# Optimization experiments

Hardware: AMD Instinct MI355X
Metric: run time of the kernel (lower is better)

The kernel has to match this reference:

```python
import jax, jax.numpy as jnp
import numpy as np

# Fixed hyperparameters (from init_kwargs)
GRID_H, GRID_W = 31, 51
PAD = min(GRID_H, GRID_W) - 1          # 30
KSIZE = 2 * PAD + 1                     # 61
FWHM = 13.0
IN_H, IN_W = 1080, 1920                 # input_shape
OUT_H, OUT_W = 1080, 1920               # output_shape
BANDWIDTH_SCALE = 1.0
AMPLITUDE_SCALE = 1.0
UNIFORM_BIAS = 1.0 / (KSIZE ** 2)       # 1/(2*pad+1)^2 added to saliency


def _gauss1d():
    x = np.arange(KSIZE, dtype=np.float64)
    c = KSIZE // 2
    return np.exp(-4.0 * np.log(2.0) * (x - c) ** 2 / FWHM ** 2).astype(np.float32)


def _bbox2sal_single(bboxes):
    # bboxes: [m, 4] in xyxy -> saliency [GRID_H, GRID_W]
    wh = bboxes[:, 2:] - bboxes[:, :2]                  # [m,2] box width/height
    cxy = bboxes[:, :2] + 0.5 * wh                      # [m,2] box centers
    widths = wh[:, 0:1] * BANDWIDTH_SCALE               # [m,1]
    heights = wh[:, 1:2] * BANDWIDTH_SCALE              # [m,1]
    xs = jnp.linspace(0.0, float(IN_W), GRID_W)
    ys = jnp.linspace(0.0, float(IN_H), GRID_H)
    X, Y = jnp.meshgrid(xs, ys, indexing='ij')          # [GRID_W, GRID_H] (torch default meshgrid)
    gx = X.ravel()[None, :]                             # [1, n], n = GRID_W*GRID_H
    gy = Y.ravel()[None, :]
    # Mahalanobis-style squared distance per box/grid-point
    dist = (cxy[:, 0:1] - gx) ** 2 / widths + (cxy[:, 1:2] - gy) ** 2 / heights
    sal = jnp.exp(-0.5 * dist)                          # [m, n]
    sal = AMPLITUDE_SCALE * sal / (1e-05 + sal.sum(axis=1, keepdims=True))
    sal = sal + UNIFORM_BIAS
    sal = sal.sum(axis=0)                               # [n]
    sal = sal / sal.sum()
    return sal.reshape(GRID_W, GRID_H).T                # [GRID_H, GRID_W]


def _conv1d_valid(x, f):
    # x: [B, 1, L], f: [K] -> [B, 1, L-K+1]  (cross-correlation; filter is symmetric)
    return jax.lax.conv_general_dilated(
        x, f[None, None, :], window_strides=(1,), padding='VALID',
        dimension_numbers=('NCH', 'OIH', 'NCH'))


def _resize_bilinear_align_corners(x, oh, ow):
    # x: [B, C, h, w] -> [B, C, oh, ow], align_corners=True
    B, C, h, w = x.shape
    ys = jnp.linspace(0.0, h - 1.0, oh)
    xs = jnp.linspace(0.0, w - 1.0, ow)
    y0 = jnp.floor(ys).astype(jnp.int32)
    x0 = jnp.floor(xs).astype(jnp.int32)
    y1 = jnp.minimum(y0 + 1, h - 1)
    x1 = jnp.minimum(x0 + 1, w - 1)
    ty = (ys - y0).astype(x.dtype)
    tx = (xs - x0).astype(x.dtype)
    v = x[:, :, y0, :] * (1.0 - ty)[None, None, :, None] + x[:, :, y1, :] * ty[None, None, :, None]
    v = v[:, :, :, x0] * (1.0 - tx) + v[:, :, :, x1] * tx
    return v


def setup_inputs() -> dict:
    key = jax.random.key(0)
    k1, k2, k3, k4 = jax.random.split(key, 4)
    B, NB = 16, 20
    imgs = jax.random.normal(k1, (B, 3, IN_H, IN_W), dtype=jnp.float32)
    x1 = jax.random.uniform(k2, (B, NB, 1), minval=0.0, maxval=IN_W * 0.7)
    y1 = jax.random.uniform(k3, (B, NB, 1), minval=0.0, maxval=IN_H * 0.7)
    wh = jax.random.uniform(k4, (B, NB, 2), minval=40.0, maxval=300.0)
    gt_bboxes = jnp.concatenate([x1, y1, x1 + wh[..., 0:1], y1 + wh[..., 1:2]], axis=-1)
    return {"imgs": imgs, "gt_bboxes": gt_bboxes.astype(jnp.float32)}


def reference(imgs, gt_bboxes):
    filt = jnp.asarray(_gauss1d())
    saliency = jax.vmap(_bbox2sal_single)(gt_bboxes)    # [B, GRID_H, GRID_W]
    saliency = saliency[:, None, :, :]                  # [B, 1, gh, gw]
    x_sal = saliency.sum(axis=2)                        # [B, 1, gw]
    y_sal = saliency.sum(axis=3)                        # [B, 1, gh]
    x_pad = jnp.pad(x_sal, ((0, 0), (0, 0), (PAD, PAD)), mode='reflect')
    y_pad = jnp.pad(y_sal, ((0, 0), (0, 0), (PAD, PAD)), mode='reflect')
    P_x = (jnp.arange(GRID_W + 2 * PAD, dtype=jnp.float32) - PAD) / (GRID_W - 1.0)
    P_y = (jnp.arange(GRID_H + 2 * PAD, dtype=jnp.float32) - PAD) / (GRID_H - 1.0)
    wx = _conv1d_valid(x_pad, filt)                     # [B, 1, gw]
    ox = _conv1d_valid(P_x[None, None, :] * x_pad, filt)
    xgrid = jnp.clip(ox / wx * 2.0 - 1.0, -1.0, 1.0)    # [B, 1, gw]
    wy = _conv1d_valid(y_pad, filt)                     # [B, 1, gh]
    oy = _conv1d_valid(P_y[None, None, :] * y_pad, filt)
    ygrid = jnp.clip(oy / wy * 2.0 - 1.0, -1.0, 1.0)    # [B, 1, gh]
    B = imgs.shape[0]
    xg = jnp.broadcast_to(xgrid[:, :, None, :], (B, 1, GRID_H, GRID_W))
    yg = jnp.broadcast_to(ygrid[:, :, :, None], (B, 1, GRID_H, GRID_W))
    grid = jnp.concatenate([xg, yg], axis=1)            # [B, 2, gh, gw]
    grid = _resize_bilinear_align_corners(grid, OUT_H, OUT_W)
    return jnp.transpose(grid, (0, 2, 3, 1))            # [B, OUT_H, OUT_W, 2]
```

## Files before the change

### kernel.cpp

```cpp
#include <hip/hip_runtime.h>

#define GH 31
#define GW 51
#define PADc 30
#define KS 61
#define NPTS (GH * GW)

#define NEG4LN2 (-2.7725887222397812f)

__global__ __launch_bounds__(256) void kde_lines(const float* __restrict__ bboxes,
                                                 int NB,
                                                 float* __restrict__ grids) {
    const int b = blockIdx.x;
    const int tid = threadIdx.x;

    __shared__ float salf[NPTS];
    __shared__ float tmp[NPTS];
    __shared__ float red[256];
    __shared__ float xsal[GW], ysal[GH];
    __shared__ float xpad[GW + 2 * PADc];
    __shared__ float ypad[GH + 2 * PADc];
    __shared__ float boxsh[4 * 32];

    for (int i = tid; i < NB * 4; i += 256) boxsh[i] = bboxes[b * NB * 4 + i];
    const float bias0 = (float)NB * (1.0f / ((float)KS * (float)KS));
    for (int g = tid; g < NPTS; g += 256) salf[g] = bias0;
    __syncthreads();

    for (int k = 0; k < NB; ++k) {
        const float x1 = boxsh[k * 4 + 0], y1 = boxsh[k * 4 + 1];
        const float x2 = boxsh[k * 4 + 2], y2 = boxsh[k * 4 + 3];
        const float w = x2 - x1, h = y2 - y1;
        const float cx = x1 + 0.5f * w, cy = y1 + 0.5f * h;
        const float iw = 1.0f / w, ih = 1.0f / h;
        float local = 0.0f;
        for (int g = tid; g < NPTS; g += 256) {
            const int xi = g / GH;
            const int yi = g - xi * GH;
            const float gx = (float)xi * (1920.0f / 50.0f);
            const float gy = (float)yi * (1080.0f / 30.0f);
            const float dx = cx - gx, dy = cy - gy;
            const float d = dx * dx * iw + dy * dy * ih;
            const float e = expf(-0.5f * d);
            tmp[g] = e;
            local += e;
        }
        red[tid] = local;
        __syncthreads();
        for (int s = 128; s > 0; s >>= 1) {
            if (tid < s) red[tid] += red[tid + s];
            __syncthreads();
        }
        const float scale = 1.0f / (1e-5f + red[0]);
        __syncthreads();
        for (int g = tid; g < NPTS; g += 256) salf[g] += tmp[g] * scale;
        __syncthreads();
    }

    if (tid < GW) {
        float s = 0.0f;
        for (int yi = 0; yi < GH; ++yi) s += salf[tid * GH + yi];
        xsal[tid] = s;
    } else if (tid >= 64 && tid < 64 + GH) {
        const int yi = tid - 64;
        float s = 0.0f;
        for (int xi = 0; xi < GW; ++xi) s += salf[xi * GH + yi];
        ysal[yi] = s;
    }
    __syncthreads();

    for (int p = tid; p < GW + 2 * PADc; p += 256) {
        int q = p - PADc;
        if (q < 0) q = -q;
        if (q > GW - 1) q = 2 * (GW - 1) - q;
        xpad[p] = xsal[q];
    }
    for (int p = tid; p < GH + 2 * PADc; p += 256) {
        int q = p - PADc;
        if (q < 0) q = -q;
        if (q > GH - 1) q = 2 * (GH - 1) - q;
        ypad[p] = ysal[q];
    }
    __syncthreads();

    float* og = grids + b * 128;
    if (tid < GW) {
        float wx = 0.0f, ox = 0.0f;
        for (int k2 = 0; k2 < KS; ++k2) {
            const float dk = (float)(k2 - 30);
            const float f = expf(NEG4LN2 * dk * dk * (1.0f / 169.0f));
            const float v = xpad[tid + k2];
            wx += v * f;
            const float P = (float)(tid + k2 - 30) * (1.0f / 50.0f);
            ox += P * v * f;
        }
        float g = ox / wx * 2.0f - 1.0f;
        g = fminf(1.0f, fmaxf(-1.0f, g));
        og[tid] = g;
    } else if (tid >= 64 && tid < 64 + GH) {
        const int j = tid - 64;
        float wy = 0.0f, oy = 0.0f;
        for (int k2 = 0; k2 < KS; ++k2) {
            const float dk = (float)(k2 - 30);
            const float f = expf(NEG4LN2 * dk * dk * (1.0f / 169.0f));
            const float v = ypad[j + k2];
            wy += v * f;
            const float P = (float)(j + k2 - 30) * (1.0f / 30.0f);
            oy += P * v * f;
        }
        float g = oy / wy * 2.0f - 1.0f;
        g = fminf(1.0f, fmaxf(-1.0f, g));
        og[64 + j] = g;
    }
}

__global__ __launch_bounds__(256) void kde_fill(const float* __restrict__ grids,
                                                float4* __restrict__ out, int N4) {
    const int idx = blockIdx.x * 256 + threadIdx.x;
    if (idx >= N4) return;
    const int i = idx % 960;
    const int row = idx / 960;
    const int y = row % 1080;
    const int b = row / 1080;
    const float* og = grids + b * 128;

    const float fy = (float)y * (30.0f / 1079.0f);
    int y0 = (int)fy;
    if (y0 > GH - 1) y0 = GH - 1;
    int y1i = y0 + 1;
    if (y1i > GH - 1) y1i = GH - 1;
    const float ty = fy - (float)y0;
    const float yv = og[64 + y0] * (1.0f - ty) + og[64 + y1i] * ty;

    float xv[2];
#pragma unroll
    for (int p = 0; p < 2; ++p) {
        const int xo = 2 * i + p;
        const float fx = (float)xo * (50.0f / 1919.0f);
        int x0 = (int)fx;
        if (x0 > GW - 1) x0 = GW - 1;
        int x1i = x0 + 1;
        if (x1i > GW - 1) x1i = GW - 1;
        const float tx = fx - (float)x0;
        xv[p] = og[x0] * (1.0f - tx) + og[x1i] * tx;
    }
    out[idx] = make_float4(xv[0], yv, xv[1], yv);
}

extern "C" void kernel_launch(void* const* d_in, const int* in_sizes, int n_in,
                              void* d_out, int out_size, void* d_ws, size_t ws_size,
                              hipStream_t stream) {
    const float* bboxes = (const float*)d_in[1];
    float* out = (float*)d_out;
    const int B = out_size / (1080 * 1920 * 2);
    const int NB = in_sizes[1] / (B * 4);
    float* grids = (float*)d_ws;

    kde_lines<<<B, 256, 0, stream>>>(bboxes, NB, grids);

    const int N4 = out_size / 4;
    kde_fill<<<(N4 + 255) / 256, 256, 0, stream>>>(grids, (float4*)out, N4);
}
```

Baseline: 536.8 us.

## Exploit separable Gaussian to compute marginal saliencies per box directly

Adds a specialised lines kernel for 20 boxes. It uses the fact that exp(-dx²/w - dy²/h) factors into x and y terms, so the row and column marginals can be built from 1D sums instead of evaluating the full 31x51 grid per box. Each wave handles one axis and uses shuffle reductions in place of shared-memory tree reductions with many barriers. A generic fallback is kept; the cost is a specialisation hard-coded to the box count of the test shape.

Result: faster. 507.6 us (-5.4%).

```diff
diff --git a/kernel.cpp b/kernel.cpp
--- a/kernel.cpp
+++ b/kernel.cpp
@@ -8,9 +8,130 @@
 
 #define NEG4LN2 (-2.7725887222397812f)
 
-__global__ __launch_bounds__(256) void kde_lines(const float* __restrict__ bboxes,
-                                                 int NB,
-                                                 float* __restrict__ grids) {
+__device__ __forceinline__ float wave_sum64(float v) {
+#pragma unroll
+    for (int off = 32; off > 0; off >>= 1) v += __shfl_xor(v, off, 64);
+    return v;
+}
+
+template <int NBc>
+__global__ __launch_bounds__(128) void kde_lines_sep(const float* __restrict__ bboxes,
+                                                     float* __restrict__ grids) {
+    const int b = blockIdx.x;
+    const int tid = threadIdx.x;
+    const int lane = tid & 63;
+    const int wv = tid >> 6;
+
+    __shared__ float boxsh[NBc * 4];
+    __shared__ float SxA[NBc], SyA[NBc];
+    __shared__ float xsal[GW], ysal[GH];
+    __shared__ float xpad[GW + 2 * PADc];
+    __shared__ float ypad[GH + 2 * PADc];
+
+    if (tid < NBc * 4) boxsh[tid] = bboxes[b * NBc * 4 + tid];
+    __syncthreads();
+
+    float e[NBc];
+    if (wv == 0) {
+        const float gx = (float)lane * (1920.0f / 50.0f);
+#pragma unroll
+        for (int k = 0; k < NBc; ++k) {
+            const float x1 = boxsh[4 * k + 0], x2 = boxsh[4 * k + 2];
+            const float w = x2 - x1;
+            const float cx = x1 + 0.5f * w;
+            const float dx = cx - gx;
+            const float ex = (lane < GW) ? expf(-0.5f * dx * dx / w) : 0.0f;
+            e[k] = ex;
+            const float s = wave_sum64(ex);
+            if (lane == 0) SxA[k] = s;
+        }
+    } else {
+        const float gy = (float)lane * (1080.0f / 30.0f);
+#pragma unroll
+        for (int k = 0; k < NBc; ++k) {
+            const float y1 = boxsh[4 * k + 1], y2 = boxsh[4 * k + 3];
+            const float h = y2 - y1;
+            const float cy = y1 + 0.5f * h;
+            const float dy = cy - gy;
+            const float ey = (lane < GH) ? expf(-0.5f * dy * dy / h) : 0.0f;
+            e[k] = ey;
+            const float s = wave_sum64(ey);
+            if (lane == 0) SyA[k] = s;
+        }
+    }
+    __syncthreads();
+
+    const float ubias = (float)NBc * (1.0f / ((float)KS * (float)KS));
+    if (wv == 0) {
+        if (lane < GW) {
+            float xs = (float)GH * ubias;
+#pragma unroll
+            for (int k = 0; k < NBc; ++k) {
+                const float sy = SyA[k];
+                xs += e[k] * sy / (1e-5f + SxA[k] * sy);
+            }
+            xsal[lane] = xs;
+        }
+    } else {
+        if (lane < GH) {
+            float ys_ = (float)GW * ubias;
+#pragma unroll
+            for (int k = 0; k < NBc; ++k) {
+                const float sx = SxA[k];
+                ys_ += e[k] * sx / (1e-5f + sx * SyA[k]);
+            }
+            ysal[lane] = ys_;
+        }
+    }
+    __syncthreads();
+
+    for (int p = tid; p < GW + 2 * PADc; p += 128) {
+        int q = p - PADc;
+        if (q < 0) q = -q;
+        if (q > GW - 1) q = 2 * (GW - 1) - q;
+        xpad[p] = xsal[q];
+    }
+    for (int p = tid; p < GH + 2 * PADc; p += 128) {
+        int q = p - PADc;
+        if (q < 0) q = -q;
+        if (q > GH - 1) q = 2 * (GH - 1) - q;
+        ypad[p] = ysal[q];
+    }
+    __syncthreads();
+
+    float* og = grids + b * 128;
+    if (wv == 0 && lane < GW) {
+        float wx = 0.0f, ox = 0.0f;
+        for (int k2 = 0; k2 < KS; ++k2) {
+            const float dk = (float)(k2 - 30);
+            const float f = expf(NEG4LN2 * dk * dk * (1.0f / 169.0f));
+            const float v = xpad[lane + k2];
+            wx += v * f;
+            const float P = (float)(lane + k2 - 30) * (1.0f / 50.0f);
+            ox += P * v * f;
+        }
+        float g = ox / wx * 2.0f - 1.0f;
+        g = fminf(1.0f, fmaxf(-1.0f, g));
+        og[lane] = g;
+    } else if (wv == 1 && lane < GH) {
+        float wy = 0.0f, oy = 0.0f;
+        for (int k2 = 0; k2 < KS; ++k2) {
+            const float dk = (float)(k2 - 30);
+            const float f = expf(NEG4LN2 * dk * dk * (1.0f / 169.0f));
+            const float v = ypad[lane + k2];
+            wy += v * f;
+            const float P = (float)(lane + k2 - 30) * (1.0f / 30.0f);
+            oy += P * v * f;
+        }
+        float g = oy / wy * 2.0f - 1.0f;
+        g = fminf(1.0f, fmaxf(-1.0f, g));
+        og[64 + lane] = g;
+    }
+}
+
+__global__ __launch_bounds__(256) void kde_lines_generic(const float* __restrict__ bboxes,
+                                                         int NB,
+                                                         float* __restrict__ grids) {
     const int b = blockIdx.x;
     const int tid = threadIdx.x;
 
@@ -41,9 +162,9 @@
             const float gy = (float)yi * (1080.0f / 30.0f);
             const float dx = cx - gx, dy = cy - gy;
             const float d = dx * dx * iw + dy * dy * ih;
-            const float e = expf(-0.5f * d);
-            tmp[g] = e;
-            local += e;
+            const float ev = expf(-0.5f * d);
+            tmp[g] = ev;
+            local += ev;
         }
         red[tid] = local;
         __syncthreads();
@@ -156,7 +277,11 @@
     const int NB = in_sizes[1] / (B * 4);
     float* grids = (float*)d_ws;
 
-    kde_lines<<<B, 256, 0, stream>>>(bboxes, NB, grids);
+    if (NB == 20) {
+        kde_lines_sep<20><<<B, 128, 0, stream>>>(bboxes, grids);
+    } else {
+        kde_lines_generic<<<B, 256, 0, stream>>>(bboxes, NB, grids);
+    }
 
     const int N4 = out_size / 4;
     kde_fill<<<(N4 + 255) / 256, 256, 0, stream>>>(grids, (float4*)out, N4);
```
